# Performance work log

Measured on AMD Instinct MI355X. Metric: run time of the kernel, lower is better.

The kernel has to match this reference:

```python
import jax, jax.numpy as jnp
import numpy as np

B, N, H = 16, 4096, 2048

def setup_inputs() -> dict:
    key = jax.random.key(0)
    k1, k2 = jax.random.split(key)
    outputs = jax.random.normal(k1, (B, N, H), dtype=jnp.float32)
    last_h = jax.random.normal(k2, (B, H), dtype=jnp.float32)
    return {"outputs": outputs, "last_h": last_h}

def reference(outputs, last_h):
    # q: [B, H] single query; k = v = outputs: [B, N, H]
    scale = jnp.asarray(outputs.shape[-1] ** 0.5, dtype=outputs.dtype)
    # logits: [B, N]
    logits = jnp.einsum("bh,bnh->bn", last_h, outputs) / scale
    attn = jax.nn.softmax(logits, axis=-1)          # [B, N]
    ctx = jnp.einsum("bn,bnh->bh", attn, outputs)   # [B, H]
    return (ctx, attn)
```

## Files before the change

kernel.cpp:

```cpp
#include <hip/hip_runtime.h>
#include <math.h>

constexpr int B = 16;
constexpr int N = 4096;
constexpr int H = 2048;

constexpr int BLOCKS_PER_BATCH = 32;
constexpr int WAVES_PER_BLOCK  = 4;
constexpr int WAVES_PER_BATCH  = BLOCKS_PER_BATCH * WAVES_PER_BLOCK;
constexpr int ROWS_PER_WAVE    = N / WAVES_PER_BATCH;
constexpr int F4_PER_ROW       = H / 4;
constexpr int F4_PER_LANE      = F4_PER_ROW / 64;

__device__ __constant__ float kInvScale = 0.022097086912079608f;

__global__ __launch_bounds__(256, 2) void attn_pass1(
    const float* __restrict__ outs,
    const float* __restrict__ last_h,
    float* __restrict__ ws_logits,
    float* __restrict__ ws_m,
    float* __restrict__ ws_l,
    float* __restrict__ ws_ctx)
{
    const int b    = blockIdx.x / BLOCKS_PER_BATCH;
    const int blk  = blockIdx.x % BLOCKS_PER_BATCH;
    const int wave = threadIdx.x >> 6;
    const int lane = threadIdx.x & 63;
    const int wid  = blk * WAVES_PER_BLOCK + wave;
    const int row0 = wid * ROWS_PER_WAVE;

    const float4* q4 = reinterpret_cast<const float4*>(last_h + (size_t)b * H);
    float4 q[F4_PER_LANE];
#pragma unroll
    for (int j = 0; j < F4_PER_LANE; ++j) q[j] = q4[lane + 64 * j];

    float4 ctx[F4_PER_LANE];
#pragma unroll
    for (int j = 0; j < F4_PER_LANE; ++j) ctx[j] = make_float4(0.f, 0.f, 0.f, 0.f);
    float m = -INFINITY;
    float l = 0.f;

    const float4* krow = reinterpret_cast<const float4*>(outs) +
                         ((size_t)b * N + row0) * F4_PER_ROW;

    for (int r = 0; r < ROWS_PER_WAVE; ++r) {
        float4 k[F4_PER_LANE];
#pragma unroll
        for (int j = 0; j < F4_PER_LANE; ++j) k[j] = krow[lane + 64 * j];
        krow += F4_PER_ROW;

        float s = 0.f;
#pragma unroll
        for (int j = 0; j < F4_PER_LANE; ++j)
            s += k[j].x * q[j].x + k[j].y * q[j].y + k[j].z * q[j].z + k[j].w * q[j].w;
#pragma unroll
        for (int off = 32; off > 0; off >>= 1) s += __shfl_xor(s, off, 64);
        s *= kInvScale;

        if (lane == 0) ws_logits[(size_t)b * N + row0 + r] = s;

        if (s > m) {
            const float corr = __expf(m - s);
            l *= corr;
#pragma unroll
            for (int j = 0; j < F4_PER_LANE; ++j) {
                ctx[j].x *= corr; ctx[j].y *= corr;
                ctx[j].z *= corr; ctx[j].w *= corr;
            }
            m = s;
        }
        const float w = __expf(s - m);
        l += w;
#pragma unroll
        for (int j = 0; j < F4_PER_LANE; ++j) {
            ctx[j].x += w * k[j].x; ctx[j].y += w * k[j].y;
            ctx[j].z += w * k[j].z; ctx[j].w += w * k[j].w;
        }
    }

    const int gw = b * WAVES_PER_BATCH + wid;
    if (lane == 0) { ws_m[gw] = m; ws_l[gw] = l; }
    float4* cdst = reinterpret_cast<float4*>(ws_ctx) + (size_t)gw * F4_PER_ROW;
#pragma unroll
    for (int j = 0; j < F4_PER_LANE; ++j) cdst[lane + 64 * j] = ctx[j];
}

__global__ __launch_bounds__(256) void attn_pass2(
    const float* __restrict__ ws_logits,
    const float* __restrict__ ws_m,
    const float* __restrict__ ws_l,
    const float* __restrict__ ws_ctx,
    float* __restrict__ out_ctx,
    float* __restrict__ out_attn)
{
    __shared__ float lm[WAVES_PER_BATCH];
    __shared__ float ll[WAVES_PER_BATCH];
    __shared__ float lscale[WAVES_PER_BATCH];

    const int b   = blockIdx.x;
    const int tid = threadIdx.x;

    if (tid < WAVES_PER_BATCH) {
        lm[tid] = ws_m[b * WAVES_PER_BATCH + tid];
        ll[tid] = ws_l[b * WAVES_PER_BATCH + tid];
    }
    __syncthreads();

    float M = -INFINITY;
    for (int w = 0; w < WAVES_PER_BATCH; ++w) M = fmaxf(M, lm[w]);
    if (tid < WAVES_PER_BATCH) lscale[tid] = __expf(lm[tid] - M);
    __syncthreads();

    float L = 0.f;
    for (int w = 0; w < WAVES_PER_BATCH; ++w) L += lscale[w] * ll[w];
    const float invL = 1.f / L;

    const float4* c4 = reinterpret_cast<const float4*>(ws_ctx) +
                       (size_t)b * WAVES_PER_BATCH * F4_PER_ROW;
    float4* o4 = reinterpret_cast<float4*>(out_ctx) + (size_t)b * F4_PER_ROW;
    for (int f = tid; f < F4_PER_ROW; f += 256) {
        float4 acc = make_float4(0.f, 0.f, 0.f, 0.f);
        for (int w = 0; w < WAVES_PER_BATCH; ++w) {
            const float sc = lscale[w];
            const float4 v = c4[(size_t)w * F4_PER_ROW + f];
            acc.x += sc * v.x; acc.y += sc * v.y;
            acc.z += sc * v.z; acc.w += sc * v.w;
        }
        o4[f] = make_float4(acc.x * invL, acc.y * invL, acc.z * invL, acc.w * invL);
    }

    for (int n = tid; n < N; n += 256) {
        out_attn[(size_t)b * N + n] =
            __expf(ws_logits[(size_t)b * N + n] - M) * invL;
    }
}

extern "C" void kernel_launch(void* const* d_in, const int* in_sizes, int n_in,
                              void* d_out, int out_size, void* d_ws, size_t ws_size,
                              hipStream_t stream) {
    const float* outs   = (const float*)d_in[0];
    const float* last_h = (const float*)d_in[1];

    float* out_ctx  = (float*)d_out;
    float* out_attn = (float*)d_out + (size_t)B * H;

    float* ws        = (float*)d_ws;
    float* ws_logits = ws;
    float* ws_m      = ws_logits + (size_t)B * N;
    float* ws_l      = ws_m + (size_t)B * WAVES_PER_BATCH;
    float* ws_ctx    = ws_l + (size_t)B * WAVES_PER_BATCH;

    attn_pass1<<<B * BLOCKS_PER_BATCH, 256, 0, stream>>>(
        outs, last_h, ws_logits, ws_m, ws_l, ws_ctx);
    attn_pass2<<<B, 256, 0, stream>>>(
        ws_logits, ws_m, ws_l, ws_ctx, out_ctx, out_attn);
}
```

Before: 704.1 us.

## Double pass-1 split and parallelize combine pass across eight blocks per batch

Pass 1 now uses 64 blocks per batch (1024 blocks total) with occupancy hint 4, so each wave processes 16 rows instead of 32. Pass 2, which previously ran only 16 blocks, now launches 8 blocks per batch: four reduce the partial context vectors for a quarter of H each, using two half-block partial sums combined through shared memory, and four write the attention probabilities. The aim is to spread the memory-bound streaming and the tail combine across more CUs. The cost is twice as much partial-context workspace (256 waves per batch) to write in pass 1 and read back in pass 2, plus higher register pressure under the stricter launch bound.

```diff
diff --git a/kernel.cpp b/kernel.cpp
--- a/kernel.cpp
+++ b/kernel.cpp
@@ -5,16 +5,16 @@
 constexpr int N = 4096;
 constexpr int H = 2048;
 
-constexpr int BLOCKS_PER_BATCH = 32;
+constexpr int BLOCKS_PER_BATCH = 64;
 constexpr int WAVES_PER_BLOCK  = 4;
 constexpr int WAVES_PER_BATCH  = BLOCKS_PER_BATCH * WAVES_PER_BLOCK;
 constexpr int ROWS_PER_WAVE    = N / WAVES_PER_BATCH;
 constexpr int F4_PER_ROW       = H / 4;
 constexpr int F4_PER_LANE      = F4_PER_ROW / 64;
 
-__device__ __constant__ float kInvScale = 0.022097086912079608f;
+constexpr float kInvScale = 0.022097086912079608f;
 
-__global__ __launch_bounds__(256, 2) void attn_pass1(
+__global__ __launch_bounds__(256, 4) void attn_pass1(
     const float* __restrict__ outs,
     const float* __restrict__ last_h,
     float* __restrict__ ws_logits,
@@ -94,44 +94,60 @@
     float* __restrict__ out_attn)
 {
     __shared__ float lm[WAVES_PER_BATCH];
-    __shared__ float ll[WAVES_PER_BATCH];
     __shared__ float lscale[WAVES_PER_BATCH];
+    __shared__ float lsl[WAVES_PER_BATCH];
+    __shared__ float4 red[128];
 
-    const int b   = blockIdx.x;
-    const int tid = threadIdx.x;
+    const int bid  = blockIdx.x;
+    const int b    = bid >> 3;
+    const int part = bid & 7;
+    const int tid  = threadIdx.x;
 
-    if (tid < WAVES_PER_BATCH) {
-        lm[tid] = ws_m[b * WAVES_PER_BATCH + tid];
-        ll[tid] = ws_l[b * WAVES_PER_BATCH + tid];
-    }
+    const float mw = ws_m[b * WAVES_PER_BATCH + tid];
+    const float lw = ws_l[b * WAVES_PER_BATCH + tid];
+    lm[tid] = mw;
     __syncthreads();
 
     float M = -INFINITY;
     for (int w = 0; w < WAVES_PER_BATCH; ++w) M = fmaxf(M, lm[w]);
-    if (tid < WAVES_PER_BATCH) lscale[tid] = __expf(lm[tid] - M);
+
+    const float sc = __expf(mw - M);
+    lscale[tid] = sc;
+    lsl[tid]    = sc * lw;
     __syncthreads();
 
     float L = 0.f;
-    for (int w = 0; w < WAVES_PER_BATCH; ++w) L += lscale[w] * ll[w];
+    for (int w = 0; w < WAVES_PER_BATCH; ++w) L += lsl[w];
     const float invL = 1.f / L;
 
-    const float4* c4 = reinterpret_cast<const float4*>(ws_ctx) +
-                       (size_t)b * WAVES_PER_BATCH * F4_PER_ROW;
-    float4* o4 = reinterpret_cast<float4*>(out_ctx) + (size_t)b * F4_PER_ROW;
-    for (int f = tid; f < F4_PER_ROW; f += 256) {
+    if (part < 4) {
+        const int f  = part * 128 + (tid & 127);
+        const int wh = tid >> 7;
+        const float4* c4 = reinterpret_cast<const float4*>(ws_ctx) +
+                           (size_t)b * WAVES_PER_BATCH * F4_PER_ROW;
         float4 acc = make_float4(0.f, 0.f, 0.f, 0.f);
-        for (int w = 0; w < WAVES_PER_BATCH; ++w) {
-            const float sc = lscale[w];
+        for (int w = wh * 128; w < wh * 128 + 128; ++w) {
+            const float s = lscale[w];
             const float4 v = c4[(size_t)w * F4_PER_ROW + f];
-            acc.x += sc * v.x; acc.y += sc * v.y;
-            acc.z += sc * v.z; acc.w += sc * v.w;
+            acc.x += s * v.x; acc.y += s * v.y;
+            acc.z += s * v.z; acc.w += s * v.w;
         }
-        o4[f] = make_float4(acc.x * invL, acc.y * invL, acc.z * invL, acc.w * invL);
-    }
-
-    for (int n = tid; n < N; n += 256) {
-        out_attn[(size_t)b * N + n] =
-            __expf(ws_logits[(size_t)b * N + n] - M) * invL;
+        if (wh == 1) red[tid & 127] = acc;
+        __syncthreads();
+        if (wh == 0) {
+            const float4 o = red[tid];
+            float4* o4 = reinterpret_cast<float4*>(out_ctx) + (size_t)b * F4_PER_ROW;
+            o4[f] = make_float4((acc.x + o.x) * invL, (acc.y + o.y) * invL,
+                                (acc.z + o.z) * invL, (acc.w + o.w) * invL);
+        }
+    } else {
+        const int n0 = (part - 4) * 1024;
+#pragma unroll
+        for (int i = 0; i < 4; ++i) {
+            const int n = n0 + i * 256 + tid;
+            out_attn[(size_t)b * N + n] =
+                __expf(ws_logits[(size_t)b * N + n] - M) * invL;
+        }
     }
 }
 
@@ -152,6 +168,6 @@
 
     attn_pass1<<<B * BLOCKS_PER_BATCH, 256, 0, stream>>>(
         outs, last_h, ws_logits, ws_m, ws_l, ws_ctx);
-    attn_pass2<<<B, 256, 0, stream>>>(
+    attn_pass2<<<B * 8, 256, 0, stream>>>(
         ws_logits, ws_m, ws_l, ws_ctx, out_ctx, out_attn);
 }
```

Result: slower. 728.8 us (+3.5%).
